# Kernel optimization log

Hardware: AMD Instinct MI355X
Metric: run time of the kernel (lower is better)

The kernel has to match this reference:

```python
import jax, jax.numpy as jnp
import numpy as np

N_CAT, N_PER = 5, 20
N_NODES = N_CAT * N_PER  # 100
T, IN_DIM, H = 512, 256, 1024


def gru_seq(x, Wih, Whh, bih, bhh):
    # x: (B, T, IN). torch GRU (batch_first), returns all hidden states (B, T, H).
    B = x.shape[0]
    Hd = Whh.shape[1]
    xp = x @ Wih.T + bih  # (B, T, 3H) precomputed input projections

    def step(h, xt):
        gh = h @ Whh.T + bhh
        xr, xz, xn = jnp.split(xt, 3, axis=-1)
        hr, hz, hn = jnp.split(gh, 3, axis=-1)
        r = jax.nn.sigmoid(xr + hr)
        z = jax.nn.sigmoid(xz + hz)
        n = jnp.tanh(xn + r * hn)
        h_new = (1.0 - z) * n + z * h
        return h_new, h_new

    h0 = jnp.zeros((B, Hd), x.dtype)
    _, hs = jax.lax.scan(step, h0, jnp.swapaxes(xp, 0, 1))
    return jnp.swapaxes(hs, 0, 1)  # (B, T, H)


def attention_block(x, Wt, bt):
    # x: (B, T, D). Linear over the time axis, softmax over output-time axis.
    # w[b,u,d] = sum_t x[b,t,d] * Wt[u,t] + bt[u]
    w = jnp.einsum('btd,ut->bud', x, Wt) + bt[None, :, None]
    probs = jax.nn.softmax(w, axis=1)  # softmax over u (time) per (b, d)
    return jnp.sum(probs * x, axis=1)  # (B, D)


def gat_conv(x, edge_index, W, a_src, a_dst, bias):
    # Single-head PyG GATConv with default add_self_loops=True, neg slope 0.2.
    N = x.shape[0]
    loops = jnp.arange(N)
    src = jnp.concatenate([edge_index[0], loops])
    dst = jnp.concatenate([edge_index[1], loops])
    h = x @ W.T  # (N, D)
    alpha_s = h @ a_src  # (N,)
    alpha_d = h @ a_dst
    e = jax.nn.leaky_relu(alpha_s[src] + alpha_d[dst], negative_slope=0.2)
    # segment softmax over incoming edges per target node
    emax = jax.ops.segment_max(e, dst, num_segments=N)
    ex = jnp.exp(e - emax[dst])
    denom = jax.ops.segment_sum(ex, dst, num_segments=N)
    alpha = ex / denom[dst]
    out = jax.ops.segment_sum(alpha[:, None] * h[src], dst, num_segments=N)
    return out + bias


def setup_inputs() -> dict:
    key = jax.random.key(0)
    ks = jax.random.split(key, 24)
    s = 0.05

    def rn(k, shape):
        return jax.random.normal(k, shape, dtype=jnp.float32) * s

    # structured edge lists
    inner = []
    for c in range(N_CAT):
        for i in range(N_PER):
            for j in range(N_PER):
                if i != j:
                    inner.append((c * N_PER + i, c * N_PER + j))
    inner_edge = jnp.asarray(np.array(inner, dtype=np.int64).T)  # (2, 1900)
    outer = [(i, j) for i in range(N_CAT) for j in range(N_CAT) if i != j]
    outer_edge = jnp.asarray(np.array(outer, dtype=np.int64).T)  # (2, 20)

    return {
        'weekly_batch': jax.random.normal(ks[0], (N_NODES, T, IN_DIM), dtype=jnp.float32),
        'gru_Wih': rn(ks[1], (3 * H, IN_DIM)),
        'gru_Whh': rn(ks[2], (3 * H, H)),
        'gru_bih': rn(ks[3], (3 * H,)),
        'gru_bhh': rn(ks[4], (3 * H,)),
        'enc_att_W': rn(ks[5], (T, T)),
        'enc_att_b': rn(ks[6], (T,)),
        'pool_att_W': rn(ks[7], (N_PER, N_PER)),
        'pool_att_b': rn(ks[8], (N_PER,)),
        'inner_W': rn(ks[9], (H, H)),
        'inner_asrc': rn(ks[10], (H,)),
        'inner_adst': rn(ks[11], (H,)),
        'inner_b': rn(ks[12], (H,)),
        'cat_W': rn(ks[13], (H, H)),
        'cat_asrc': rn(ks[14], (H,)),
        'cat_adst': rn(ks[15], (H,)),
        'cat_b': rn(ks[16], (H,)),
        'fusion_W': rn(ks[17], (H, 3 * H)),
        'fusion_b': rn(ks[18], (H,)),
        'reg_W': rn(ks[19], (1, H)),
        'reg_b': rn(ks[20], (1,)),
        'cls_W': rn(ks[21], (1, H)),
        'cls_b': rn(ks[22], (1,)),
        'inner_edge': inner_edge,
        'outer_edge': outer_edge,
    }


def reference(weekly_batch, gru_Wih, gru_Whh, gru_bih, gru_bhh,
              enc_att_W, enc_att_b, pool_att_W, pool_att_b,
              inner_W, inner_asrc, inner_adst, inner_b,
              cat_W, cat_asrc, cat_adst, cat_b,
              fusion_W, fusion_b, reg_W, reg_b, cls_W, cls_b,
              inner_edge, outer_edge):
    # SequenceEncoder: GRU + (eval-mode dropout = identity) + attention pooling
    seq = gru_seq(weekly_batch.reshape(-1, T, IN_DIM), gru_Wih, gru_Whh, gru_bih, gru_bhh)
    v = attention_block(seq, enc_att_W, enc_att_b)  # (100, H)

    # inner GAT over all 100 nodes
    inner_emb = gat_conv(v, inner_edge, inner_W, inner_asrc, inner_adst, inner_b)
    inner_emb = inner_emb.reshape(N_CAT, N_PER, H)
    vv = v.reshape(N_CAT, N_PER, H)

    # pool 20 stocks -> 1 category vector, then category-level GAT
    cat_vec = attention_block(vv, pool_att_W, pool_att_b)  # (5, H)
    cat_vec = gat_conv(cat_vec, outer_edge, cat_W, cat_asrc, cat_adst, cat_b)
    cat_exp = jnp.broadcast_to(cat_vec[:, None, :], (N_CAT, N_PER, H))

    fusion = jnp.concatenate([vv, cat_exp, inner_emb], axis=-1)  # (5, 20, 3H)
    f = jax.nn.relu(fusion @ fusion_W.T + fusion_b)
    reg_out = (f @ reg_W.T + reg_b).reshape(-1)  # (100,)
    cls_out = jax.nn.sigmoid(f @ cls_W.T + cls_b).reshape(-1)  # (100,)
    return reg_out, cls_out
```

## Files before the change

kernel.cpp:

```cpp
#include <hip/hip_runtime.h>
#include <hip/hip_bf16.h>


typedef __bf16 bf16x8 __attribute__((ext_vector_type(8)));
typedef float  floatx4 __attribute__((ext_vector_type(4)));
typedef int    intx4  __attribute__((ext_vector_type(4)));

struct US8 { unsigned short u[8]; };

__device__ __forceinline__ unsigned short f2bf(float f) {
  unsigned u = __builtin_bit_cast(unsigned, f);
  u += 0x7fffu + ((u >> 16) & 1u);
  return (unsigned short)(u >> 16);
}
__device__ __forceinline__ float bf2f(unsigned short h) {
  return __builtin_bit_cast(float, ((unsigned)h) << 16);
}
__device__ __forceinline__ float sigm(float x) { return 1.f / (1.f + __expf(-x)); }

__device__ __forceinline__ void bar_lds() {
  asm volatile("s_waitcnt lgkmcnt(0)" ::: "memory");
  __builtin_amdgcn_s_barrier();
  asm volatile("" ::: "memory");
}

static const size_t OF_XBF   = 0;
static const size_t OF_HIST  = 26214400;
static const size_t OF_ENCW  = 131277824;
static const size_t OF_V     = 131802112;
static const size_t OF_HIN   = 132211712;
static const size_t OF_IEMB  = 132621312;
static const size_t OF_CATV  = 133030912;
static const size_t OF_CATH  = 133051392;
static const size_t OF_CATO  = 133071872;
static const size_t OF_FBUF  = 133092352;
static const size_t OF_FOUT  = 134321152;
static const size_t OF_FLAGS = 134730752;

__global__ void f2bf_kernel(const float* __restrict__ src, unsigned short* __restrict__ dst, int n4) {
  int i = blockIdx.x * 256 + threadIdx.x;
  if (i < n4) {
    float4 v = ((const float4*)src)[i];
    ushort4 o;
    o.x = f2bf(v.x); o.y = f2bf(v.y); o.z = f2bf(v.z); o.w = f2bf(v.w);
    ((ushort4*)dst)[i] = o;
  }
}

__global__ void encw_pack(const float* __restrict__ src, unsigned short* __restrict__ dst) {
  int idx = blockIdx.x * 256 + threadIdx.x;
  int kk   = idx >> 11;
  int rem  = idx & 2047;
  int lane = rem & 63;
  int ut   = rem >> 6;
  int u = ut * 16 + (lane & 15);
  int k = kk * 32 + (lane >> 4) * 8;
  const float* sp = src + (size_t)u * 512 + k;
  float4 f0 = *(const float4*)sp;
  float4 f1 = *(const float4*)(sp + 4);
  US8 o;
  o.u[0] = f2bf(f0.x); o.u[1] = f2bf(f0.y); o.u[2] = f2bf(f0.z); o.u[3] = f2bf(f0.w);
  o.u[4] = f2bf(f1.x); o.u[5] = f2bf(f1.y); o.u[6] = f2bf(f1.z); o.u[7] = f2bf(f1.w);
  *(intx4*)(dst + (size_t)idx * 8) = __builtin_bit_cast(intx4, o);
}

#define GRU_LDS 163136
__global__ void __launch_bounds__(320) gru_recur(
    const unsigned short* __restrict__ xbf,
    const float* __restrict__ Whh, const float* __restrict__ Wih,
    const float* __restrict__ bih, const float* __restrict__ bhh,
    unsigned short* hist, int* flags)
{
  extern __shared__ char smem[];
  unsigned* hbf  = (unsigned*)smem;
  unsigned short* Bw  = (unsigned short*)smem;
  float* biasl = (float*)(smem + 122880);
  float* ghp   = (float*)(smem + 123136);
  float* hfp   = (float*)(smem + 161536);

  const int tid  = threadIdx.x;
  const int lane = tid & 63;
  const int w    = tid >> 6;
  const int wg   = blockIdx.x;
  const int g    = wg >> 6;
  const int s    = wg & 63;
  const int gb   = g * 25;
  const int myq  = s >> 4;

  for (int o = tid; o < 7680; o += 320) {
    int kk, ln; const float* sp; unsigned short* dst;
    if (o < 5120) {
      int q = o >= 2560; int rem = o - q * 2560;
      kk = rem >> 6; ln = rem & 63;
      int l = ln & 15, ksub = ln >> 4, j = s * 16 + l;
      int k = kk * 32 + ksub * 8;
      sp = (k < 1024) ? (Whh + (size_t)(q * 1024 + j) * 1024 + k)
                      : (Wih + (size_t)(q * 1024 + j) * 256 + (k - 1024));
      dst = Bw + ((size_t)((q * 40 + kk) * 64 + ln)) * 8;
    } else if (o < 7168) {
      int o2 = o - 5120; kk = o2 >> 6; ln = o2 & 63;
      int l = ln & 15, ksub = ln >> 4, j = s * 16 + l;
      sp = Whh + (size_t)(2048 + j) * 1024 + kk * 32 + ksub * 8;
      dst = Bw + (size_t)(5120 + kk * 64 + ln) * 8;
    } else {
      int o3 = o - 7168; kk = o3 >> 6; ln = o3 & 63;
      int l = ln & 15, ksub = ln >> 4, j = s * 16 + l;
      sp = Wih + (size_t)(2048 + j) * 256 + kk * 32 + ksub * 8;
      dst = Bw + (size_t)(7168 + kk * 64 + ln) * 8;
    }
    float4 f0 = *(const float4*)sp;
    float4 f1 = *(const float4*)(sp + 4);
    dst[0] = f2bf(f0.x); dst[1] = f2bf(f0.y); dst[2] = f2bf(f0.z); dst[3] = f2bf(f0.w);
    dst[4] = f2bf(f1.x); dst[5] = f2bf(f1.y); dst[6] = f2bf(f1.z); dst[7] = f2bf(f1.w);
  }
  if (tid < 16) {
    int j = s * 16 + tid;
    biasl[tid]      = bih[j]        + bhh[j];
    biasl[16 + tid] = bih[1024 + j] + bhh[1024 + j];
    biasl[32 + tid] = bhh[2048 + j];
    biasl[48 + tid] = bih[2048 + j];
  }
  for (int i = tid; i < 400; i += 320) hfp[i] = 0.f;
  __syncthreads();

  bf16x8 Breg[24];
  #pragma unroll
  for (int lk = 0; lk < 8; lk++) {
    int kk = w * 8 + lk;
    Breg[lk * 3 + 0] = __builtin_bit_cast(bf16x8, *(const intx4*)(Bw + (size_t)((kk)      * 64 + lane) * 8));
    Breg[lk * 3 + 1] = __builtin_bit_cast(bf16x8, *(const intx4*)(Bw + (size_t)((40 + kk) * 64 + lane) * 8));
    const unsigned short* np = (w < 4)
        ? (Bw + (size_t)(5120 + kk * 64 + lane) * 8)
        : (Bw + (size_t)(7168 + (kk - 32) * 64 + lane) * 8);
    Breg[lk * 3 + 2] = __builtin_bit_cast(bf16x8, *(const intx4*)np);
  }

  const int kf_x = (lane >> 4) * 8;
  size_t baseA[2], rowx[2];
  #pragma unroll
  for (int mt = 0; mt < 2; mt++) {
    int m = mt * 16 + (lane & 15);
    int bb = (m < 25) ? m : 24;
    baseA[mt] = (size_t)((g * 64 + (lane >> 5)) * 400 + bb * 16 + ((lane >> 4) & 1) * 8);
    rowx[mt]  = (size_t)(gb + bb) * 512 * 256;
  }

  const int* pollline = flags + (wg * 4 + w) * 16;

  for (int t = 0; t < 512; t++) {
    if (w < 4) {
      for (;;) {
        int f = __hip_atomic_load(pollline + (lane & 15), __ATOMIC_RELAXED, __HIP_MEMORY_SCOPE_AGENT);
        if (__all(f >= t)) break;
      }
      asm volatile("" ::: "memory");
    }

    const unsigned short* hrow = hist + (size_t)t * 102400;
    floatx4 acc[2][3];
    #pragma unroll
    for (int mt = 0; mt < 2; mt++)
      #pragma unroll
      for (int gg = 0; gg < 3; gg++) acc[mt][gg] = floatx4{0.f, 0.f, 0.f, 0.f};

    #pragma unroll
    for (int lk = 0; lk < 8; lk++) {
      int kk = w * 8 + lk;
      #pragma unroll
      for (int mt = 0; mt < 2; mt++) {
        const unsigned short* ap = (w < 4)
            ? (hrow + baseA[mt] + (size_t)kk * 800)
            : (xbf + rowx[mt] + (size_t)t * 256 + (kk - 32) * 32 + kf_x);
        bf16x8 a = __builtin_bit_cast(bf16x8, *(const intx4*)ap);
        acc[mt][0] = __builtin_amdgcn_mfma_f32_16x16x32_bf16(a, Breg[lk * 3 + 0], acc[mt][0], 0, 0, 0);
        acc[mt][1] = __builtin_amdgcn_mfma_f32_16x16x32_bf16(a, Breg[lk * 3 + 1], acc[mt][1], 0, 0, 0);
        acc[mt][2] = __builtin_amdgcn_mfma_f32_16x16x32_bf16(a, Breg[lk * 3 + 2], acc[mt][2], 0, 0, 0);
      }
    }

    {
      int base = (lane & 15) * 20 + (lane >> 4) * 4;
      #pragma unroll
      for (int mt = 0; mt < 2; mt++)
        #pragma unroll
        for (int gg = 0; gg < 3; gg++)
          *(floatx4*)(ghp + (size_t)((w * 2 + mt) * 3 + gg) * 320 + base) = acc[mt][gg];
    }
    bar_lds();

    if (tid < 256) {
      int lp = tid >> 5, b = tid & 31;
      if (b < 25) {
        int mt2 = b >> 4, rr = b & 15;
        unsigned packed = 0;
        #pragma unroll
        for (int ii = 0; ii < 2; ii++) {
          int l = lp * 2 + ii;
          int off = l * 20 + rr;
          float ghr = 0.f, ghz = 0.f, ghnh = 0.f, ghnx;
          #pragma unroll
          for (int ww = 0; ww < 4; ww++) {
            const float* gq = ghp + (size_t)((ww * 2 + mt2) * 3) * 320 + off;
            ghr += gq[0]; ghz += gq[320]; ghnh += gq[640];
          }
          { const float* gq = ghp + (size_t)((4 * 2 + mt2) * 3) * 320 + off;
            ghr += gq[0]; ghz += gq[320]; ghnx = gq[640]; }
          float r = sigm(ghr + biasl[l]);
          float z = sigm(ghz + biasl[16 + l]);
          float nv = ghnx + biasl[48 + l] + r * (ghnh + biasl[32 + l]);
          nv = fminf(fmaxf(nv, -15.f), 15.f);
          float e2 = __expf(-2.f * nv);
          float n = (1.f - e2) / (1.f + e2);
          float ho = hfp[l * 25 + b];
          float hn = (1.f - z) * n + z * ho;
          hfp[l * 25 + b] = hn;
          packed |= ((unsigned)f2bf(hn)) << (16 * ii);
        }
        hbf[b * 8 + lp] = packed;
      }
    }
    bar_lds();

    if (w == 4) {
      if (lane < 50) {
        int b = lane >> 1, hs = lane & 1;
        intx4 d = *(const intx4*)&hbf[b * 8 + hs * 4];
        unsigned long long addr = (unsigned long long)(hist + (size_t)(t + 1) * 102400
                                  + (size_t)((g * 64 + s) * 400 + b * 16 + hs * 8));
        asm volatile("global_store_dwordx4 %0, %1, off sc0 sc1" :: "v"(addr), "v"(d) : "memory");
      }
      if (t < 511) {
        asm volatile("s_waitcnt vmcnt(0)" ::: "memory");
        __hip_atomic_store(flags + ((g * 64 + lane) * 4 + myq) * 16 + (s & 15), t + 1,
                           __ATOMIC_RELAXED, __HIP_MEMORY_SCOPE_AGENT);
      }
    }
  }
}

#define ATT_LDS 68096
__global__ void __launch_bounds__(512) att_pool(
    const unsigned short* __restrict__ hist,
    const unsigned short* __restrict__ encw,
    const float* __restrict__ encb,
    float* __restrict__ vout)
{
  extern __shared__ char smem[];
  unsigned short* Bs = (unsigned short*)smem;
  float* red  = (float*)(smem + 65536);
  float* cmax = (float*)(smem + 65536 + 2048);
  float* csum = (float*)(smem + 65536 + 2048 + 256);

  const int tid = threadIdx.x, w = tid >> 6, lane = tid & 63;
  const int q = lane >> 4, col = lane & 15;
  const int n0 = blockIdx.x * 64;
  const int bg = n0 >> 10, d0 = n0 & 1023;
  const int gA = bg / 25, rA = bg - gA * 25;

  for (int ii = 0; ii < 8; ii++) {
    int c = tid + 512 * ii;
    int t = c >> 3, dd = c & 7;
    int sA = (d0 >> 4) + (dd >> 1), hsA = dd & 1;
    intx4 li = *(const intx4*)(hist + (size_t)(t + 1) * 102400
                             + (size_t)((gA * 64 + sA) * 400 + rA * 16 + hsA * 8));
    US8 u8 = __builtin_bit_cast(US8, li);
    int kstep = t >> 5, ksub = (t >> 3) & 3, i = t & 7;
    int ntile = dd >> 1, nc0 = (dd & 1) * 8;
    unsigned short* dst = Bs + ((size_t)((kstep * 4 + ntile) * 64 + ksub * 16 + nc0)) * 8 + i;
    #pragma unroll
    for (int jj = 0; jj < 8; jj++) dst[jj * 8] = u8.u[jj];
  }
  __syncthreads();

  floatx4 acc[4][4];
  #pragma unroll
  for (int mi = 0; mi < 4; mi++)
    #pragma unroll
    for (int ni = 0; ni < 4; ni++) acc[mi][ni] = floatx4{0.f, 0.f, 0.f, 0.f};

  #pragma unroll 2
  for (int kk = 0; kk < 16; kk++) {
    bf16x8 af[4];
    #pragma unroll
    for (int mi = 0; mi < 4; mi++) {
      af[mi] = __builtin_bit_cast(bf16x8,
          *(const intx4*)(encw + ((size_t)((kk * 32 + (w * 4 + mi)) * 64 + lane)) * 8));
    }
    #pragma unroll
    for (int ni = 0; ni < 4; ni++) {
      bf16x8 bf = __builtin_bit_cast(bf16x8, *(const intx4*)(Bs + (size_t)((kk * 4 + ni) * 64 + lane) * 8));
      #pragma unroll
      for (int mi = 0; mi < 4; mi++)
        acc[mi][ni] = __builtin_amdgcn_mfma_f32_16x16x32_bf16(af[mi], bf, acc[mi][ni], 0, 0, 0);
    }
  }

  #pragma unroll
  for (int mi = 0; mi < 4; mi++) {
    int ub = (w * 4 + mi) * 16 + q * 4;
    float b0 = encb[ub], b1 = encb[ub + 1], b2 = encb[ub + 2], b3 = encb[ub + 3];
    #pragma unroll
    for (int ni = 0; ni < 4; ni++) {
      acc[mi][ni][0] += b0; acc[mi][ni][1] += b1; acc[mi][ni][2] += b2; acc[mi][ni][3] += b3;
    }
  }
  #pragma unroll
  for (int ni = 0; ni < 4; ni++) {
    float m = -1e30f;
    #pragma unroll
    for (int mi = 0; mi < 4; mi++)
      #pragma unroll
      for (int r = 0; r < 4; r++) m = fmaxf(m, acc[mi][ni][r]);
    m = fmaxf(m, __shfl_xor(m, 16)); m = fmaxf(m, __shfl_xor(m, 32));
    red[w * 64 + ni * 16 + col] = m;
  }
  __syncthreads();
  if (tid < 64) {
    float m = red[tid];
    for (int w2 = 1; w2 < 8; w2++) m = fmaxf(m, red[w2 * 64 + tid]);
    cmax[tid] = m;
  }
  __syncthreads();
  #pragma unroll
  for (int ni = 0; ni < 4; ni++) {
    float cm = cmax[ni * 16 + col];
    float sum = 0.f;
    #pragma unroll
    for (int mi = 0; mi < 4; mi++)
      #pragma unroll
      for (int r = 0; r < 4; r++) {
        float e = __expf(acc[mi][ni][r] - cm);
        acc[mi][ni][r] = e; sum += e;
      }
    sum += __shfl_xor(sum, 16); sum += __shfl_xor(sum, 32);
    red[w * 64 + ni * 16 + col] = sum;
  }
  __syncthreads();
  if (tid < 64) {
    float sm = 0.f;
    for (int w2 = 0; w2 < 8; w2++) sm += red[w2 * 64 + tid];
    csum[tid] = sm;
  }
  __syncthreads();
  #pragma unroll
  for (int ni = 0; ni < 4; ni++) {
    float p = 0.f;
    #pragma unroll
    for (int mi = 0; mi < 4; mi++) {
      int u0 = (w * 4 + mi) * 16 + q * 4;
      int ks = u0 >> 5, ksb = (u0 >> 3) & 3, i0 = u0 & 7;
      const unsigned short* hp = Bs + (size_t)((ks * 4 + ni) * 64 + ksb * 16 + col) * 8 + i0;
      p += acc[mi][ni][0] * bf2f(hp[0]) + acc[mi][ni][1] * bf2f(hp[1])
         + acc[mi][ni][2] * bf2f(hp[2]) + acc[mi][ni][3] * bf2f(hp[3]);
    }
    p += __shfl_xor(p, 16); p += __shfl_xor(p, 32);
    red[w * 64 + ni * 16 + col] = p;
  }
  __syncthreads();
  if (tid < 64) {
    float p = 0.f;
    for (int w2 = 0; w2 < 8; w2++) p += red[w2 * 64 + tid];
    vout[n0 + tid] = p / csum[tid];
  }
}

__global__ void gemm_bt(const float* __restrict__ A, const float* __restrict__ B,
                        float* __restrict__ C, int M, int N, int K,
                        const float* __restrict__ bias, int relu)
{
  __shared__ float Al[16][33];
  __shared__ float Bl[64][33];
  int tx = threadIdx.x;
  int nb = blockIdx.x, mb = blockIdx.y;
  int n = nb * 64 + (tx & 63);
  int mq = tx >> 6;
  float acc[4] = {0.f, 0.f, 0.f, 0.f};
  for (int k0 = 0; k0 < K; k0 += 32) {
    for (int e = tx; e < 512; e += 256) {
      int r = e >> 5, c = e & 31; int m = mb * 16 + r;
      Al[r][c] = (m < M) ? A[(size_t)m * K + k0 + c] : 0.f;
    }
    for (int e = tx; e < 2048; e += 256) {
      int r = e >> 5, c = e & 31;
      Bl[r][c] = B[(size_t)(nb * 64 + r) * K + k0 + c];
    }
    __syncthreads();
    int nn = tx & 63;
    #pragma unroll 8
    for (int c = 0; c < 32; c++) {
      float bv = Bl[nn][c];
      #pragma unroll
      for (int i = 0; i < 4; i++) acc[i] += Al[mq * 4 + i][c] * bv;
    }
    __syncthreads();
  }
  #pragma unroll
  for (int i = 0; i < 4; i++) {
    int m = mb * 16 + mq * 4 + i;
    if (m < M && n < N) {
      float r = acc[i] + (bias ? bias[n] : 0.f);
      if (relu) r = fmaxf(r, 0.f);
      C[(size_t)m * N + n] = r;
    }
  }
}

__global__ void gemm_fuse(const float* __restrict__ v, const float* __restrict__ cato,
                          const float* __restrict__ iemb, const float* __restrict__ B,
                          float* __restrict__ C, const float* __restrict__ bias)
{
  __shared__ float Al[16][33];
  __shared__ float Bl[64][33];
  int tx = threadIdx.x;
  int nb = blockIdx.x, mb = blockIdx.y;
  int n = nb * 64 + (tx & 63);
  int mq = tx >> 6;
  float acc[4] = {0.f, 0.f, 0.f, 0.f};
  for (int k0 = 0; k0 < 3072; k0 += 32) {
    for (int e = tx; e < 512; e += 256) {
      int r = e >> 5, c = e & 31; int m = mb * 16 + r;
      float aval = 0.f;
      if (m < 100) {
        int k = k0 + c;
        if (k < 1024)       aval = v[(size_t)m * 1024 + k];
        else if (k < 2048)  aval = cato[(size_t)(m / 20) * 1024 + (k - 1024)];
        else                aval = iemb[(size_t)m * 1024 + (k - 2048)];
      }
      Al[r][c] = aval;
    }
    for (int e = tx; e < 2048; e += 256) {
      int r = e >> 5, c = e & 31;
      Bl[r][c] = B[(size_t)(nb * 64 + r) * 3072 + k0 + c];
    }
    __syncthreads();
    int nn = tx & 63;
    #pragma unroll 8
    for (int c = 0; c < 32; c++) {
      float bv = Bl[nn][c];
      #pragma unroll
      for (int i = 0; i < 4; i++) acc[i] += Al[mq * 4 + i][c] * bv;
    }
    __syncthreads();
  }
  #pragma unroll
  for (int i = 0; i < 4; i++) {
    int m = mb * 16 + mq * 4 + i;
    if (m < 100) {
      float r = fmaxf(acc[i] + bias[n], 0.f);
      C[(size_t)m * 1024 + n] = r;
    }
  }
}

template <int NN>
__global__ void gat_scores(const float* __restrict__ h, const float* __restrict__ asrc,
                           const float* __restrict__ adst, float* __restrict__ P)
{
  __shared__ float asd[2][NN];
  int c = blockIdx.x, tx = threadIdx.x;
  int wid = tx >> 6, lane = tx & 63;
  for (int idx = wid; idx < 2 * NN; idx += 4) {
    int which = idx >= NN; int j = which ? idx - NN : idx;
    const float* av = which ? adst : asrc;
    float p = 0.f;
    for (int k = lane; k < 1024; k += 64) p += h[(size_t)(c * NN + j) * 1024 + k] * av[k];
    for (int m = 32; m; m >>= 1) p += __shfl_xor(p, m);
    if (lane == 0) asd[which][j] = p;
  }
  __syncthreads();
  if (tx < NN) {
    int i = tx; float mx = -1e30f; float e[NN];
    #pragma unroll
    for (int j = 0; j < NN; j++) {
      float x = asd[0][j] + asd[1][i];
      x = (x < 0.f) ? 0.2f * x : x;
      e[j] = x; mx = fmaxf(mx, x);
    }
    float s = 0.f;
    #pragma unroll
    for (int j = 0; j < NN; j++) { e[j] = __expf(e[j] - mx); s += e[j]; }
    #pragma unroll
    for (int j = 0; j < NN; j++) P[(size_t)(c * NN + i) * NN + j] = e[j] / s;
  }
}

template <int NN>
__global__ void gat_agg(const float* __restrict__ h, const float* __restrict__ P,
                        const float* __restrict__ bias, float* __restrict__ out)
{
  int gid = blockIdx.x * 256 + threadIdx.x;
  int i = gid >> 10, d = gid & 1023;
  int c = i / NN, il = i - c * NN;
  float s = 0.f;
  #pragma unroll
  for (int j = 0; j < NN; j++)
    s += P[(size_t)(c * NN + il) * NN + j] * h[(size_t)(c * NN + j) * 1024 + d];
  out[(size_t)i * 1024 + d] = s + bias[d];
}

__global__ void pool_att(const float* __restrict__ v, const float* __restrict__ pW,
                         const float* __restrict__ pb, float* __restrict__ catv)
{
  __shared__ float W[400]; __shared__ float bsh[20];
  int tx = threadIdx.x;
  for (int i = tx; i < 400; i += 256) W[i] = pW[i];
  if (tx < 20) bsh[tx] = pb[tx];
  __syncthreads();
  int gid = blockIdx.x * 256 + tx;
  int c = gid >> 10, d = gid & 1023;
  float vals[20];
  #pragma unroll
  for (int t = 0; t < 20; t++) vals[t] = v[(size_t)(c * 20 + t) * 1024 + d];
  float wv[20]; float mx = -1e30f;
  #pragma unroll
  for (int u = 0; u < 20; u++) {
    float s = bsh[u];
    #pragma unroll
    for (int t = 0; t < 20; t++) s += vals[t] * W[u * 20 + t];
    wv[u] = s; mx = fmaxf(mx, s);
  }
  float sum = 0.f, out = 0.f;
  #pragma unroll
  for (int u = 0; u < 20; u++) { float e = __expf(wv[u] - mx); sum += e; out += e * vals[u]; }
  catv[gid] = out / sum;
}

__global__ void heads(const float* __restrict__ f, const float* __restrict__ rw,
                      const float* __restrict__ rb, const float* __restrict__ cw,
                      const float* __restrict__ cb, float* __restrict__ out)
{
  int b = blockIdx.x * 4 + (threadIdx.x >> 6);
  int lane = threadIdx.x & 63;
  float pr = 0.f, pc = 0.f;
  for (int k = lane; k < 1024; k += 64) {
    float x = f[(size_t)b * 1024 + k];
    pr += x * rw[k]; pc += x * cw[k];
  }
  for (int m = 32; m; m >>= 1) { pr += __shfl_xor(pr, m); pc += __shfl_xor(pc, m); }
  if (lane == 0) {
    out[b] = pr + rb[0];
    out[100 + b] = sigm(pc + cb[0]);
  }
}

extern "C" void kernel_launch(void* const* d_in, const int* in_sizes, int n_in,
                              void* d_out, int out_size, void* d_ws, size_t ws_size,
                              hipStream_t stream)
{
  const float* x     = (const float*)d_in[0];
  const float* Wih   = (const float*)d_in[1];
  const float* Whh   = (const float*)d_in[2];
  const float* bih   = (const float*)d_in[3];
  const float* bhh   = (const float*)d_in[4];
  const float* encW  = (const float*)d_in[5];
  const float* encb  = (const float*)d_in[6];
  const float* poolW = (const float*)d_in[7];
  const float* poolb = (const float*)d_in[8];
  const float* innW  = (const float*)d_in[9];
  const float* innas = (const float*)d_in[10];
  const float* innad = (const float*)d_in[11];
  const float* innb  = (const float*)d_in[12];
  const float* catW  = (const float*)d_in[13];
  const float* catas = (const float*)d_in[14];
  const float* catad = (const float*)d_in[15];
  const float* catb  = (const float*)d_in[16];
  const float* fusW  = (const float*)d_in[17];
  const float* fusb  = (const float*)d_in[18];
  const float* regW  = (const float*)d_in[19];
  const float* regb  = (const float*)d_in[20];
  const float* clsW  = (const float*)d_in[21];
  const float* clsb  = (const float*)d_in[22];
  float* out = (float*)d_out;
  char* ws = (char*)d_ws;

  unsigned short* xbf  = (unsigned short*)(ws + OF_XBF);
  unsigned short* hist = (unsigned short*)(ws + OF_HIST);
  int*            flg  = (int*)(ws + OF_FLAGS);
  unsigned short* ewbf = (unsigned short*)(ws + OF_ENCW);
  float* v    = (float*)(ws + OF_V);
  float* hin  = (float*)(ws + OF_HIN);
  float* iemb = (float*)(ws + OF_IEMB);
  float* catv = (float*)(ws + OF_CATV);
  float* cath = (float*)(ws + OF_CATH);
  float* cato = (float*)(ws + OF_CATO);
  float* P20  = (float*)(ws + OF_FBUF);
  float* P5   = (float*)(ws + OF_FBUF + 16384);
  float* fout = (float*)(ws + OF_FOUT);

  (void)hipFuncSetAttribute((const void*)gru_recur, hipFuncAttributeMaxDynamicSharedMemorySize, GRU_LDS);
  (void)hipFuncSetAttribute((const void*)att_pool,  hipFuncAttributeMaxDynamicSharedMemorySize, ATT_LDS);

  (void)hipMemsetAsync(hist, 0, 204800, stream);
  (void)hipMemsetAsync(flg, 0, 65536, stream);

  f2bf_kernel<<<12800, 256, 0, stream>>>(x, xbf, 13107200 / 4);
  encw_pack<<<128, 256, 0, stream>>>(encW, ewbf);

  gru_recur<<<256, 320, GRU_LDS, stream>>>(xbf, Whh, Wih, bih, bhh, hist, flg);
  att_pool<<<1600, 512, ATT_LDS, stream>>>(hist, ewbf, encb, v);

  gemm_bt<<<dim3(16, 7), 256, 0, stream>>>(v, innW, hin, 100, 1024, 1024, nullptr, 0);
  gat_scores<20><<<5, 256, 0, stream>>>(hin, innas, innad, P20);
  gat_agg<20><<<400, 256, 0, stream>>>(hin, P20, innb, iemb);
  pool_att<<<20, 256, 0, stream>>>(v, poolW, poolb, catv);
  gemm_bt<<<dim3(16, 1), 256, 0, stream>>>(catv, catW, cath, 5, 1024, 1024, nullptr, 0);
  gat_scores<5><<<1, 256, 0, stream>>>(cath, catas, catad, P5);
  gat_agg<5><<<20, 256, 0, stream>>>(cath, P5, catb, cato);
  gemm_fuse<<<dim3(16, 7), 256, 0, stream>>>(v, cato, iemb, fusW, fout, fusb);
  heads<<<25, 256, 0, stream>>>(fout, regW, regb, clsW, clsb, out);

  (void)in_sizes; (void)n_in; (void)out_size; (void)ws_size;
}
```

Before: 4.124 ms.

## Fuse init, GAT score/aggregate, and pooling launches into fewer kernels

Merges the bf16 conversion, encoder weight packing and two memsets into one init kernel, fuses GAT score and aggregation kernels (recomputing scores per block) and combines the inner GAT with category pooling into a single launch. The intent is to cut kernel launch overhead and intermediate P buffer round-trips. In exchange, each GAT block now redundantly recomputes the attention score dot products.

```diff
diff --git a/kernel.cpp b/kernel.cpp
--- a/kernel.cpp
+++ b/kernel.cpp
@@ -33,35 +33,42 @@
 static const size_t OF_CATV  = 133030912;
 static const size_t OF_CATH  = 133051392;
 static const size_t OF_CATO  = 133071872;
-static const size_t OF_FBUF  = 133092352;
 static const size_t OF_FOUT  = 134321152;
 static const size_t OF_FLAGS = 134730752;
 
-__global__ void f2bf_kernel(const float* __restrict__ src, unsigned short* __restrict__ dst, int n4) {
-  int i = blockIdx.x * 256 + threadIdx.x;
-  if (i < n4) {
-    float4 v = ((const float4*)src)[i];
+__global__ void init_kernel(const float* __restrict__ x, unsigned short* __restrict__ xbf,
+                            const float* __restrict__ encW, unsigned short* __restrict__ ewbf,
+                            unsigned short* __restrict__ hist, int* __restrict__ flags)
+{
+  int b = blockIdx.x, tid = threadIdx.x;
+  if (b < 12800) {
+    int i = b * 256 + tid;
+    float4 v = ((const float4*)x)[i];
     ushort4 o;
     o.x = f2bf(v.x); o.y = f2bf(v.y); o.z = f2bf(v.z); o.w = f2bf(v.w);
-    ((ushort4*)dst)[i] = o;
-  }
-}
-
-__global__ void encw_pack(const float* __restrict__ src, unsigned short* __restrict__ dst) {
-  int idx = blockIdx.x * 256 + threadIdx.x;
-  int kk   = idx >> 11;
-  int rem  = idx & 2047;
-  int lane = rem & 63;
-  int ut   = rem >> 6;
-  int u = ut * 16 + (lane & 15);
-  int k = kk * 32 + (lane >> 4) * 8;
-  const float* sp = src + (size_t)u * 512 + k;
-  float4 f0 = *(const float4*)sp;
-  float4 f1 = *(const float4*)(sp + 4);
-  US8 o;
-  o.u[0] = f2bf(f0.x); o.u[1] = f2bf(f0.y); o.u[2] = f2bf(f0.z); o.u[3] = f2bf(f0.w);
-  o.u[4] = f2bf(f1.x); o.u[5] = f2bf(f1.y); o.u[6] = f2bf(f1.z); o.u[7] = f2bf(f1.w);
-  *(intx4*)(dst + (size_t)idx * 8) = __builtin_bit_cast(intx4, o);
+    ((ushort4*)xbf)[i] = o;
+  } else if (b < 12928) {
+    int idx = (b - 12800) * 256 + tid;
+    int kk   = idx >> 11;
+    int rem  = idx & 2047;
+    int lane = rem & 63;
+    int ut   = rem >> 6;
+    int u = ut * 16 + (lane & 15);
+    int k = kk * 32 + (lane >> 4) * 8;
+    const float* sp = encW + (size_t)u * 512 + k;
+    float4 f0 = *(const float4*)sp;
+    float4 f1 = *(const float4*)(sp + 4);
+    US8 o;
+    o.u[0] = f2bf(f0.x); o.u[1] = f2bf(f0.y); o.u[2] = f2bf(f0.z); o.u[3] = f2bf(f0.w);
+    o.u[4] = f2bf(f1.x); o.u[5] = f2bf(f1.y); o.u[6] = f2bf(f1.z); o.u[7] = f2bf(f1.w);
+    *(intx4*)(ewbf + (size_t)idx * 8) = __builtin_bit_cast(intx4, o);
+  } else if (b < 12978) {
+    size_t off = (size_t)(b - 12928) * 4096 + (size_t)tid * 16;
+    *(intx4*)((char*)hist + off) = intx4{0, 0, 0, 0};
+  } else {
+    size_t off = (size_t)(b - 12978) * 4096 + (size_t)tid * 16;
+    *(intx4*)((char*)flags + off) = intx4{0, 0, 0, 0};
+  }
 }
 
 #define GRU_LDS 163136
@@ -452,77 +459,100 @@
   }
 }
 
-template <int NN>
-__global__ void gat_scores(const float* __restrict__ h, const float* __restrict__ asrc,
-                           const float* __restrict__ adst, float* __restrict__ P)
-{
-  __shared__ float asd[2][NN];
-  int c = blockIdx.x, tx = threadIdx.x;
+__global__ void mid_kernel(const float* __restrict__ hin, const float* __restrict__ iasrc,
+                           const float* __restrict__ iadst, const float* __restrict__ ibias,
+                           float* __restrict__ iemb,
+                           const float* __restrict__ v, const float* __restrict__ pW,
+                           const float* __restrict__ pb, float* __restrict__ catv)
+{
+  __shared__ float asd[2][20];
+  __shared__ float W[400];
+  __shared__ float bsh[20];
+  int b = blockIdx.x, tx = threadIdx.x;
+  if (b < 400) {
+    int gid = b * 256 + tx;
+    int i = gid >> 10, d = gid & 1023;
+    int c = i / 20, il = i - c * 20;
+    int wid = tx >> 6, lane = tx & 63;
+    for (int idx = wid; idx < 40; idx += 4) {
+      int which = idx >= 20; int j = which ? idx - 20 : idx;
+      const float* av = which ? iadst : iasrc;
+      float p = 0.f;
+      for (int k = lane; k < 1024; k += 64) p += hin[(size_t)(c * 20 + j) * 1024 + k] * av[k];
+      for (int m = 32; m; m >>= 1) p += __shfl_xor(p, m);
+      if (lane == 0) asd[which][j] = p;
+    }
+    __syncthreads();
+    float e[20]; float mx = -1e30f;
+    #pragma unroll
+    for (int j = 0; j < 20; j++) {
+      float xv = asd[0][j] + asd[1][il];
+      xv = (xv < 0.f) ? 0.2f * xv : xv;
+      e[j] = xv; mx = fmaxf(mx, xv);
+    }
+    float s = 0.f;
+    #pragma unroll
+    for (int j = 0; j < 20; j++) { e[j] = __expf(e[j] - mx); s += e[j]; }
+    float agg = 0.f;
+    #pragma unroll
+    for (int j = 0; j < 20; j++) agg += (e[j] / s) * hin[(size_t)(c * 20 + j) * 1024 + d];
+    iemb[(size_t)i * 1024 + d] = agg + ibias[d];
+  } else {
+    for (int i = tx; i < 400; i += 256) W[i] = pW[i];
+    if (tx < 20) bsh[tx] = pb[tx];
+    __syncthreads();
+    int gid = (b - 400) * 256 + tx;
+    int c = gid >> 10, d = gid & 1023;
+    float vals[20];
+    #pragma unroll
+    for (int t = 0; t < 20; t++) vals[t] = v[(size_t)(c * 20 + t) * 1024 + d];
+    float wv[20]; float mx = -1e30f;
+    #pragma unroll
+    for (int u = 0; u < 20; u++) {
+      float s = bsh[u];
+      #pragma unroll
+      for (int t = 0; t < 20; t++) s += vals[t] * W[u * 20 + t];
+      wv[u] = s; mx = fmaxf(mx, s);
+    }
+    float sum = 0.f, out = 0.f;
+    #pragma unroll
+    for (int u = 0; u < 20; u++) { float e = __expf(wv[u] - mx); sum += e; out += e * vals[u]; }
+    catv[gid] = out / sum;
+  }
+}
+
+__global__ void gat5_kernel(const float* __restrict__ cath, const float* __restrict__ casrc,
+                            const float* __restrict__ cadst, const float* __restrict__ cbias,
+                            float* __restrict__ cato)
+{
+  __shared__ float asd[2][5];
+  int b = blockIdx.x, tx = threadIdx.x;
+  int gid = b * 256 + tx;
+  int i = gid >> 10, d = gid & 1023;
   int wid = tx >> 6, lane = tx & 63;
-  for (int idx = wid; idx < 2 * NN; idx += 4) {
-    int which = idx >= NN; int j = which ? idx - NN : idx;
-    const float* av = which ? adst : asrc;
+  for (int idx = wid; idx < 10; idx += 4) {
+    int which = idx >= 5; int j = which ? idx - 5 : idx;
+    const float* av = which ? cadst : casrc;
     float p = 0.f;
-    for (int k = lane; k < 1024; k += 64) p += h[(size_t)(c * NN + j) * 1024 + k] * av[k];
+    for (int k = lane; k < 1024; k += 64) p += cath[(size_t)j * 1024 + k] * av[k];
     for (int m = 32; m; m >>= 1) p += __shfl_xor(p, m);
     if (lane == 0) asd[which][j] = p;
   }
   __syncthreads();
-  if (tx < NN) {
-    int i = tx; float mx = -1e30f; float e[NN];
-    #pragma unroll
-    for (int j = 0; j < NN; j++) {
-      float x = asd[0][j] + asd[1][i];
-      x = (x < 0.f) ? 0.2f * x : x;
-      e[j] = x; mx = fmaxf(mx, x);
-    }
-    float s = 0.f;
-    #pragma unroll
-    for (int j = 0; j < NN; j++) { e[j] = __expf(e[j] - mx); s += e[j]; }
-    #pragma unroll
-    for (int j = 0; j < NN; j++) P[(size_t)(c * NN + i) * NN + j] = e[j] / s;
-  }
-}
-
-template <int NN>
-__global__ void gat_agg(const float* __restrict__ h, const float* __restrict__ P,
-                        const float* __restrict__ bias, float* __restrict__ out)
-{
-  int gid = blockIdx.x * 256 + threadIdx.x;
-  int i = gid >> 10, d = gid & 1023;
-  int c = i / NN, il = i - c * NN;
+  float e[5]; float mx = -1e30f;
+  #pragma unroll
+  for (int j = 0; j < 5; j++) {
+    float xv = asd[0][j] + asd[1][i];
+    xv = (xv < 0.f) ? 0.2f * xv : xv;
+    e[j] = xv; mx = fmaxf(mx, xv);
+  }
   float s = 0.f;
   #pragma unroll
-  for (int j = 0; j < NN; j++)
-    s += P[(size_t)(c * NN + il) * NN + j] * h[(size_t)(c * NN + j) * 1024 + d];
-  out[(size_t)i * 1024 + d] = s + bias[d];
-}
-
-__global__ void pool_att(const float* __restrict__ v, const float* __restrict__ pW,
-                         const float* __restrict__ pb, float* __restrict__ catv)
-{
-  __shared__ float W[400]; __shared__ float bsh[20];
-  int tx = threadIdx.x;
-  for (int i = tx; i < 400; i += 256) W[i] = pW[i];
-  if (tx < 20) bsh[tx] = pb[tx];
-  __syncthreads();
-  int gid = blockIdx.x * 256 + tx;
-  int c = gid >> 10, d = gid & 1023;
-  float vals[20];
-  #pragma unroll
-  for (int t = 0; t < 20; t++) vals[t] = v[(size_t)(c * 20 + t) * 1024 + d];
-  float wv[20]; float mx = -1e30f;
-  #pragma unroll
-  for (int u = 0; u < 20; u++) {
-    float s = bsh[u];
-    #pragma unroll
-    for (int t = 0; t < 20; t++) s += vals[t] * W[u * 20 + t];
-    wv[u] = s; mx = fmaxf(mx, s);
-  }
-  float sum = 0.f, out = 0.f;
-  #pragma unroll
-  for (int u = 0; u < 20; u++) { float e = __expf(wv[u] - mx); sum += e; out += e * vals[u]; }
-  catv[gid] = out / sum;
+  for (int j = 0; j < 5; j++) { e[j] = __expf(e[j] - mx); s += e[j]; }
+  float agg = 0.f;
+  #pragma unroll
+  for (int j = 0; j < 5; j++) agg += (e[j] / s) * cath[(size_t)j * 1024 + d];
+  cato[(size_t)i * 1024 + d] = agg + cbias[d];
 }
 
 __global__ void heads(const float* __restrict__ f, const float* __restrict__ rw,
@@ -583,29 +613,20 @@
   float* catv = (float*)(ws + OF_CATV);
   float* cath = (float*)(ws + OF_CATH);
   float* cato = (float*)(ws + OF_CATO);
-  float* P20  = (float*)(ws + OF_FBUF);
-  float* P5   = (float*)(ws + OF_FBUF + 16384);
   float* fout = (float*)(ws + OF_FOUT);
 
   (void)hipFuncSetAttribute((const void*)gru_recur, hipFuncAttributeMaxDynamicSharedMemorySize, GRU_LDS);
   (void)hipFuncSetAttribute((const void*)att_pool,  hipFuncAttributeMaxDynamicSharedMemorySize, ATT_LDS);
 
-  (void)hipMemsetAsync(hist, 0, 204800, stream);
-  (void)hipMemsetAsync(flg, 0, 65536, stream);
-
-  f2bf_kernel<<<12800, 256, 0, stream>>>(x, xbf, 13107200 / 4);
-  encw_pack<<<128, 256, 0, stream>>>(encW, ewbf);
+  init_kernel<<<12994, 256, 0, stream>>>(x, xbf, encW, ewbf, hist, flg);
 
   gru_recur<<<256, 320, GRU_LDS, stream>>>(xbf, Whh, Wih, bih, bhh, hist, flg);
   att_pool<<<1600, 512, ATT_LDS, stream>>>(hist, ewbf, encb, v);
 
   gemm_bt<<<dim3(16, 7), 256, 0, stream>>>(v, innW, hin, 100, 1024, 1024, nullptr, 0);
-  gat_scores<20><<<5, 256, 0, stream>>>(hin, innas, innad, P20);
-  gat_agg<20><<<400, 256, 0, stream>>>(hin, P20, innb, iemb);
-  pool_att<<<20, 256, 0, stream>>>(v, poolW, poolb, catv);
+  mid_kernel<<<420, 256, 0, stream>>>(hin, innas, innad, innb, iemb, v, poolW, poolb, catv);
   gemm_bt<<<dim3(16, 1), 256, 0, stream>>>(catv, catW, cath, 5, 1024, 1024, nullptr, 0);
-  gat_scores<5><<<1, 256, 0, stream>>>(cath, catas, catad, P5);
-  gat_agg<5><<<20, 256, 0, stream>>>(cath, P5, catb, cato);
+  gat5_kernel<<<20, 256, 0, stream>>>(cath, catas, catad, catb, cato);
   gemm_fuse<<<dim3(16, 7), 256, 0, stream>>>(v, cato, iemb, fusW, fout, fusb);
   heads<<<25, 256, 0, stream>>>(fout, regW, regb, clsW, clsb, out);
 
```

Result: no change. 4.120 ms (-0.1%).
